# Performance work log

Hardware: AMD Instinct MI355X
Metric: run time of the kernel (lower is better)

## Reference

```python
import jax, jax.numpy as jnp
import numpy as np

NEG_SLOPE = 0.2  # PyG GATConv default leaky_relu slope


def gat_conv(h_in, src, dst, W, a_src, a_dst, b, N):
    # h_in: [N, Fin]; src/dst: [E] (self-loops already appended)
    h = h_in @ W                      # [N, Fout]
    alpha_src = h @ a_src             # [N]
    alpha_dst = h @ a_dst             # [N]
    e = jax.nn.leaky_relu(alpha_src[src] + alpha_dst[dst], NEG_SLOPE)  # [E]
    # segment softmax over incoming edges of each destination node
    m = jax.ops.segment_max(e, dst, num_segments=N)
    m = jnp.where(jnp.isfinite(m), m, 0.0)
    p = jnp.exp(e - m[dst])
    denom = jax.ops.segment_sum(p, dst, num_segments=N)
    alpha = p / jnp.maximum(denom[dst], 1e-16)
    out = jax.ops.segment_sum(alpha[:, None] * h[src], dst, num_segments=N)
    return out + b


def setup_inputs() -> dict:
    key = jax.random.key(0)
    ks = jax.random.split(key, 16)
    N, E, V, D, H, C, G = 100000, 1600000, 128, 50, 16, 10, 512
    x = jax.random.normal(ks[0], (N, V), dtype=jnp.float32)
    edge_index = jax.random.randint(ks[1], (2, E), 0, N, dtype=jnp.int32)
    batch = jnp.sort(jax.random.randint(ks[2], (N,), 0, G, dtype=jnp.int32))
    s = lambda fan: 1.0 / np.sqrt(fan)
    return {
        "x": x, "edge_index": edge_index, "batch": batch,
        "embedding": jax.random.normal(ks[3], (V, D), dtype=jnp.float32),
        "W1": jax.random.normal(ks[4], (D, H), dtype=jnp.float32) * s(D),
        "a_src1": jax.random.normal(ks[5], (H,), dtype=jnp.float32) * s(H),
        "a_dst1": jax.random.normal(ks[6], (H,), dtype=jnp.float32) * s(H),
        "b1": jnp.zeros((H,), dtype=jnp.float32),
        "W2": jax.random.normal(ks[7], (H, H), dtype=jnp.float32) * s(H),
        "a_src2": jax.random.normal(ks[8], (H,), dtype=jnp.float32) * s(H),
        "a_dst2": jax.random.normal(ks[9], (H,), dtype=jnp.float32) * s(H),
        "b2": jnp.zeros((H,), dtype=jnp.float32),
        "W3": jax.random.normal(ks[10], (H, C), dtype=jnp.float32) * s(H),
        "a_src3": jax.random.normal(ks[11], (C,), dtype=jnp.float32) * s(C),
        "a_dst3": jax.random.normal(ks[12], (C,), dtype=jnp.float32) * s(C),
        "b3": jnp.zeros((C,), dtype=jnp.float32),
    }


def reference(x, edge_index, batch, embedding, W1, a_src1, a_dst1, b1,
              W2, a_src2, a_dst2, b2, W3, a_src3, a_dst3, b3):
    N = x.shape[0]
    G = 512  # num graphs
    # embedding lookup via argmax over one-hot-ish features
    idx = jnp.argmax(x, axis=1)
    h = embedding[idx]                               # [N, 50]
    # add self-loops once (PyG GATConv default)
    loops = jnp.arange(N, dtype=edge_index.dtype)
    src = jnp.concatenate([edge_index[0], loops])
    dst = jnp.concatenate([edge_index[1], loops])
    h = jax.nn.relu(gat_conv(h, src, dst, W1, a_src1, a_dst1, b1, N))
    # dropout: eval mode -> identity
    h = jax.nn.relu(gat_conv(h, src, dst, W2, a_src2, a_dst2, b2, N))
    h = gat_conv(h, src, dst, W3, a_src3, a_dst3, b3, N)  # [N, C]
    # global mean pool over graphs
    sums = jax.ops.segment_sum(h, batch, num_segments=G)
    cnts = jax.ops.segment_sum(jnp.ones((N,), h.dtype), batch, num_segments=G)
    pooled = sums / jnp.maximum(cnts, 1.0)[:, None]
    return jax.nn.softmax(pooled, axis=1)
```

## Files before the change

kernel.cpp:

```cpp
#include <hip/hip_runtime.h>
#include <math.h>

#define NEG_SLOPE 0.2f
#define NBUK_MAX 512

typedef float v4f __attribute__((ext_vector_type(4)));

template <int B2>
__global__ void __launch_bounds__(1024)
k_histarg(const float* __restrict__ x, const int* __restrict__ edst, int E,
          int* __restrict__ histT, int NBUK, int* __restrict__ idx, int N, int V) {
    __shared__ int sh[NBUK_MAX];
    int t = threadIdx.x;
    if ((int)blockIdx.x < B2) {
        int b = blockIdx.x;
        for (int k = t; k < NBUK; k += 1024) sh[k] = 0;
        __syncthreads();
        long long ebeg = (long long)b * E / B2, eend = (long long)(b + 1) * E / B2;
        for (long long i = ebeg + t; i < eend; i += 1024)
            atomicAdd(&sh[edst[i] >> 8], 1);
        __syncthreads();
        for (int k = t; k < NBUK; k += 1024) histT[(long long)k * B2 + b] = sh[k];
    } else {
        int node = ((int)blockIdx.x - B2) * 32 + (t >> 5);
        int lane = t & 31;
        if (node >= N) return;
        const v4f* row = (const v4f*)(x + (long long)node * V);
        float bv = -INFINITY;
        int bi = 0x7fffffff;
        int nq = V >> 2;
        for (int q = lane; q < nq; q += 32) {
            v4f v = row[q];
            int base = q << 2;
            if (v.x > bv || (v.x == bv && base     < bi)) { bv = v.x; bi = base;     }
            if (v.y > bv || (v.y == bv && base + 1 < bi)) { bv = v.y; bi = base + 1; }
            if (v.z > bv || (v.z == bv && base + 2 < bi)) { bv = v.z; bi = base + 2; }
            if (v.w > bv || (v.w == bv && base + 3 < bi)) { bv = v.w; bi = base + 3; }
        }
        for (int off = 16; off > 0; off >>= 1) {
            float ov = __shfl_down(bv, off, 32);
            int   oi = __shfl_down(bi, off, 32);
            if (ov > bv || (ov == bv && oi < bi)) { bv = ov; bi = oi; }
        }
        if (lane == 0) idx[node] = bi;
    }
}

template <int FIN, int FOUT>
__global__ void __launch_bounds__(256)
k_scan_tr(const int* __restrict__ vals, int* __restrict__ excl, int* __restrict__ bsums, int M,
          const float* __restrict__ emb, const int* __restrict__ idx,
          const float* __restrict__ W, const float* __restrict__ a_src,
          const float* __restrict__ a_dst, _Float16* __restrict__ h_t,
          float* __restrict__ asrc, float* __restrict__ adst, int N, int NB_SCAN) {
    __shared__ int s[256];
    __shared__ float sW[FIN * FOUT];
    __shared__ float sa[FOUT], sd[FOUT];
    int t = threadIdx.x;
    if ((int)blockIdx.x < NB_SCAN) {
        int i = blockIdx.x * 256 + t;
        int v = (i < M) ? vals[i] : 0;
        s[t] = v;
        __syncthreads();
        for (int off = 1; off < 256; off <<= 1) {
            int a = (t >= off) ? s[t - off] : 0;
            __syncthreads();
            s[t] += a;
            __syncthreads();
        }
        if (i < M) excl[i] = s[t] - v;
        if (t == 255) bsums[blockIdx.x] = s[255];
    } else {
        for (int i = t; i < FIN * FOUT; i += 256) sW[i] = W[i];
        if (t < FOUT) { sa[t] = a_src[t]; sd[t] = a_dst[t]; }
        __syncthreads();
        int n = ((int)blockIdx.x - NB_SCAN) * 256 + t;
        if (n >= N) return;
        float acc[FOUT];
#pragma unroll
        for (int f = 0; f < FOUT; f++) acc[f] = 0.f;
        const float* hr = emb + (long long)idx[n] * FIN;
        for (int k = 0; k < FIN; k++) {
            float v = hr[k];
#pragma unroll
            for (int f = 0; f < FOUT; f++) acc[f] += v * sW[k * FOUT + f];
        }
        float s1 = 0.f, s2 = 0.f;
        _Float16 hh[16];
#pragma unroll
        for (int f = 0; f < 16; f++) hh[f] = (_Float16)0.f;
#pragma unroll
        for (int f = 0; f < FOUT; f++) {
            hh[f] = (_Float16)acc[f];
            s1 += acc[f] * sa[f];
            s2 += acc[f] * sd[f];
        }
        uint4* dst = (uint4*)(h_t + (long long)n * 16);
        dst[0] = ((uint4*)hh)[0];
        dst[1] = ((uint4*)hh)[1];
        asrc[n] = s1;
        adst[n] = s2;
    }
}

__global__ void k_scan2(int* __restrict__ bsums, int nb) {
    __shared__ int s[2048];
    int i = threadIdx.x;
    int v0 = (i < nb) ? bsums[i] : 0;
    int v1 = (i + 1024 < nb) ? bsums[i + 1024] : 0;
    s[i] = v0;
    s[i + 1024] = v1;
    __syncthreads();
    for (int off = 1; off < 2048; off <<= 1) {
        int a0 = (i >= off) ? s[i - off] : 0;
        int a1 = (i + 1024 >= off) ? s[i + 1024 - off] : 0;
        __syncthreads();
        s[i] += a0;
        s[i + 1024] += a1;
        __syncthreads();
    }
    if (i < nb) bsums[i] = s[i] - v0;
    if (i + 1024 < nb) bsums[i + 1024] = s[i + 1024] - v1;
}

template <int B2>
__global__ void __launch_bounds__(1024)
k_scatB(const int* __restrict__ esrc, const int* __restrict__ edst, int E,
        const int* __restrict__ sexcl, const int* __restrict__ bsums,
        int* __restrict__ tmp, int NBUK) {
    __shared__ int cur[NBUK_MAX];
    int t = threadIdx.x, b = blockIdx.x;
    for (int k = t; k < NBUK; k += 1024)
        cur[k] = sexcl[(long long)k * B2 + b] + bsums[k];
    __syncthreads();
    long long ebeg = (long long)b * E / B2, eend = (long long)(b + 1) * E / B2;
    for (long long i = ebeg + t; i < eend; i += 1024) {
        int d = edst[i];
        int pos = atomicAdd(&cur[d >> 8], 1);
        tmp[pos] = ((d & 255) << 17) | esrc[i];
    }
}

template <int B2>
__global__ void __launch_bounds__(256)
k_binB(const int* __restrict__ sexcl, const int* __restrict__ bsums,
       const int* __restrict__ tmp,
       int* __restrict__ rowptr, int* __restrict__ csr_src, int N, int NBUK, int E) {
    __shared__ int cnt[256];
    __shared__ int scn[256];
    __shared__ int cur[256];
    int t = threadIdx.x, b = blockIdx.x;
    int t0 = sexcl[(long long)b * B2] + bsums[b];
    int t1 = (b + 1 < NBUK) ? (sexcl[(long long)(b + 1) * B2] + bsums[b + 1]) : E;
    cnt[t] = 0;
    __syncthreads();
    for (int i = t0 + t; i < t1; i += 256) atomicAdd(&cnt[tmp[i] >> 17], 1);
    __syncthreads();
    int v = cnt[t];
    scn[t] = v;
    __syncthreads();
    for (int off = 1; off < 256; off <<= 1) {
        int a = (t >= off) ? scn[t - off] : 0;
        __syncthreads();
        scn[t] += a;
        __syncthreads();
    }
    int base = t0 + scn[t] - v;
    int d = (b << 8) + t;
    if (d < N) rowptr[d] = base;
    cur[t] = base;
    if (d == N - 1) rowptr[N] = E;
    __syncthreads();
    for (int i = t0 + t; i < t1; i += 256) {
        int p = tmp[i];
        int pos = atomicAdd(&cur[p >> 17], 1);
        csr_src[pos] = p & 0x1FFFF;
    }
}

template <typename EPI>
__device__ __forceinline__ void gat_core(const int* __restrict__ rowptr,
                                         const int* __restrict__ csr_src,
                                         const float* __restrict__ asrc,
                                         const float* __restrict__ adst,
                                         const _Float16* __restrict__ h_t,
                                         int N, int grp, int lane, EPI epilogue) {
    int d = grp;
    int r0 = rowptr[d], r1 = rowptr[d + 1];
    float ad = adst[d];

    float e0 = asrc[d] + ad;
    e0 = (e0 >= 0.f) ? e0 : NEG_SLOPE * e0;
    float p0 = __expf(e0);
    float acc  = p0 * (float)h_t[(long long)d * 16 + lane];
    float psum = (lane == 0) ? p0 : 0.f;

    int j = r0;
    if (j < r1) {
        int myj = j + lane;
        bool valid = myj < r1;
        int s = valid ? csr_src[myj] : d;
        float a = asrc[s];
        while (true) {
            int jn = j + 16;
            int s2 = d; float a2 = 0.f; bool validn = false;
            if (jn < r1) {
                int myjn = jn + lane;
                validn = myjn < r1;
                s2 = validn ? csr_src[myjn] : d;
                a2 = asrc[s2];
            }
            float e = a + ad;
            e = (e >= 0.f) ? e : NEG_SLOPE * e;
            float p = valid ? __expf(e) : 0.f;
            psum += p;
#pragma unroll
            for (int k = 0; k < 16; k++) {
                float pk = __shfl(p, k, 16);
                int   sk = __shfl(s, k, 16);
                acc += pk * (float)h_t[(long long)sk * 16 + lane];
            }
            if (jn >= r1) break;
            j = jn; s = s2; a = a2; valid = validn;
        }
    }
    for (int off = 8; off > 0; off >>= 1) psum += __shfl_xor(psum, off, 16);
    epilogue(d, acc / fmaxf(psum, 1e-16f));
}

template <int FN>
__global__ void k_gat_ft(const int* __restrict__ rowptr, const int* __restrict__ csr_src,
                         const float* __restrict__ asrc, const float* __restrict__ adst,
                         const _Float16* __restrict__ h_t, const float* __restrict__ bias,
                         const float* __restrict__ Wn, const float* __restrict__ an_src,
                         const float* __restrict__ an_dst,
                         _Float16* __restrict__ h_next, float* __restrict__ asrc_n,
                         float* __restrict__ adst_n, int N) {
    __shared__ float sW[16 * FN];
    __shared__ float sa[FN], sd[FN], sb[16];
    for (int i = threadIdx.x; i < 16 * FN; i += blockDim.x) sW[i] = Wn[i];
    if (threadIdx.x < FN) { sa[threadIdx.x] = an_src[threadIdx.x]; sd[threadIdx.x] = an_dst[threadIdx.x]; }
    if (threadIdx.x < 16) sb[threadIdx.x] = bias[threadIdx.x];
    __syncthreads();

    int grp  = (blockIdx.x * blockDim.x + threadIdx.x) >> 4;
    int lane = threadIdx.x & 15;
    if (grp >= N) return;

    gat_core(rowptr, csr_src, asrc, adst, h_t, N, grp, lane,
        [&](int d, float v) {
            v = fmaxf(v + sb[lane], 0.f);
            float acc2 = 0.f;
#pragma unroll
            for (int k = 0; k < 16; k++) {
                float vk = __shfl(v, k, 16);
                if (lane < FN) acc2 += vk * sW[k * FN + lane];
            }
            float c1 = (lane < FN) ? acc2 * sa[lane] : 0.f;
            float c2 = (lane < FN) ? acc2 * sd[lane] : 0.f;
            for (int off = 8; off > 0; off >>= 1) {
                c1 += __shfl_xor(c1, off, 16);
                c2 += __shfl_xor(c2, off, 16);
            }
            h_next[(long long)d * 16 + lane] = (_Float16)((lane < FN) ? acc2 : 0.f);
            if (lane == 0) { asrc_n[d] = c1; adst_n[d] = c2; }
        });
}

template <int FOUT>
__global__ void k_gat_last(const int* __restrict__ rowptr, const int* __restrict__ csr_src,
                           const float* __restrict__ asrc, const float* __restrict__ adst,
                           const _Float16* __restrict__ h_t, float* __restrict__ out, int N) {
    int grp  = (blockIdx.x * blockDim.x + threadIdx.x) >> 4;
    int lane = threadIdx.x & 15;
    if (grp >= N) return;
    gat_core(rowptr, csr_src, asrc, adst, h_t, N, grp, lane,
        [&](int d, float v) {
            if (lane < FOUT) out[(long long)d * FOUT + lane] = v;
        });
}

__global__ void k_pool(const float* __restrict__ h3, const int* __restrict__ batch,
                       const float* __restrict__ b3, float* __restrict__ out, int N, int C) {
    int g = blockIdx.x;
    int lo = 0, hi = N;
    while (lo < hi) { int mid = (lo + hi) >> 1; if (batch[mid] < g) lo = mid + 1; else hi = mid; }
    int start = lo;
    hi = N;
    while (lo < hi) { int mid = (lo + hi) >> 1; if (batch[mid] < g + 1) lo = mid + 1; else hi = mid; }
    int end = lo;

    float sum[16];
    for (int f = 0; f < C; f++) sum[f] = 0.f;
    for (int n = start + threadIdx.x; n < end; n += blockDim.x) {
        const float* r = h3 + (long long)n * C;
        for (int f = 0; f < C; f++) sum[f] += r[f];
    }
    __shared__ float red[256 * 16];
    for (int f = 0; f < C; f++) red[threadIdx.x * 16 + f] = sum[f];
    __syncthreads();
    for (int str = blockDim.x / 2; str > 0; str >>= 1) {
        if ((int)threadIdx.x < str)
            for (int f = 0; f < C; f++) red[threadIdx.x * 16 + f] += red[(threadIdx.x + str) * 16 + f];
        __syncthreads();
    }
    if (threadIdx.x == 0) {
        float cnt = fmaxf((float)(end - start), 1.f);
        float vals[16];
        float mx = -INFINITY;
        for (int f = 0; f < C; f++) { vals[f] = red[f] / cnt + b3[f]; mx = fmaxf(mx, vals[f]); }
        float se = 0.f;
        for (int f = 0; f < C; f++) { vals[f] = __expf(vals[f] - mx); se += vals[f]; }
        for (int f = 0; f < C; f++) out[(long long)g * C + f] = vals[f] / se;
    }
}

extern "C" void kernel_launch(void* const* d_in, const int* in_sizes, int n_in,
                              void* d_out, int out_size, void* d_ws, size_t ws_size,
                              hipStream_t stream) {
    const float* x    = (const float*)d_in[0];
    const int*   eidx = (const int*)d_in[1];
    const int*   batch= (const int*)d_in[2];
    const float* emb  = (const float*)d_in[3];
    const float* W1   = (const float*)d_in[4];
    const float* as1  = (const float*)d_in[5];
    const float* ad1  = (const float*)d_in[6];
    const float* b1   = (const float*)d_in[7];
    const float* W2   = (const float*)d_in[8];
    const float* as2  = (const float*)d_in[9];
    const float* ad2  = (const float*)d_in[10];
    const float* b2   = (const float*)d_in[11];
    const float* W3   = (const float*)d_in[12];
    const float* as3  = (const float*)d_in[13];
    const float* ad3  = (const float*)d_in[14];
    const float* b3   = (const float*)d_in[15];

    const int H = in_sizes[5];
    const int C = in_sizes[13];
    const int D = in_sizes[4] / H;
    const int V = in_sizes[3] / D;
    const int N = in_sizes[0] / V;
    const int E = in_sizes[1] / 2;
    const int G = out_size / C;
    const int* esrc = eidx;
    const int* edst = eidx + E;
    const int NBUK = (N + 255) >> 8;
    constexpr int B2 = 256;
    const int M = NBUK * B2;

    char* w = (char*)d_ws;
    auto carve = [&](size_t bytes) {
        char* p = w;
        w += (bytes + 255) & ~(size_t)255;
        return p;
    };
    float*     as_a    = (float*)carve((size_t)N * 4);
    float*     ad_a    = (float*)carve((size_t)N * 4);
    float*     as_b    = (float*)carve((size_t)N * 4);
    float*     ad_b    = (float*)carve((size_t)N * 4);
    int*       idx     = (int*)carve((size_t)N * 4);
    int*       rowptr  = (int*)carve((size_t)(N + 1) * 4);
    int*       csr_src = (int*)carve((size_t)E * 4);
    int*       histT   = (int*)carve((size_t)M * 4);
    int*       sexcl   = (int*)carve((size_t)M * 4);
    int*       bsums   = (int*)carve(2048 * 4);
    _Float16*  hTa     = (_Float16*)carve((size_t)N * 16 * 2);
    _Float16*  hTb     = (_Float16*)carve((size_t)N * 16 * 2);
    size_t zone_bytes = ((size_t)E * 4 > (size_t)N * C * 4) ? (size_t)E * 4 : (size_t)N * C * 4;
    char*  zone = carve(zone_bytes);
    float* X0  = (float*)zone;
    int*   tmp = (int*)zone;
    (void)ws_size; (void)n_in;

    const int BT = 256;
    dim3 blk(BT);
    int gGat  = (N * 16 + BT - 1) / BT;
    int nb2   = (M + 255) / 256;
    int gArg  = (N + 31) / 32;
    int gTr   = (N + BT - 1) / BT;

    k_histarg<B2><<<B2 + gArg, dim3(1024), 0, stream>>>(x, edst, E, histT, NBUK, idx, N, V);

    k_scan_tr<50, 16><<<nb2 + gTr, blk, 0, stream>>>(histT, sexcl, bsums, M,
                                                     emb, idx, W1, as1, ad1, hTa, as_a, ad_a, N, nb2);
    k_scan2<<<1, 1024, 0, stream>>>(bsums, nb2);

    k_scatB<B2><<<B2, dim3(1024), 0, stream>>>(esrc, edst, E, sexcl, bsums, tmp, NBUK);
    k_binB<B2><<<NBUK, blk, 0, stream>>>(sexcl, bsums, tmp, rowptr, csr_src, N, NBUK, E);

    k_gat_ft<16><<<gGat, blk, 0, stream>>>(rowptr, csr_src, as_a, ad_a, hTa, b1,
                                           W2, as2, ad2, hTb, as_b, ad_b, N);

    k_gat_ft<10><<<gGat, blk, 0, stream>>>(rowptr, csr_src, as_b, ad_b, hTb, b2,
                                           W3, as3, ad3, hTa, as_a, ad_a, N);

    k_gat_last<10><<<gGat, blk, 0, stream>>>(rowptr, csr_src, as_a, ad_a, hTa, X0, N);

    k_pool<<<G, blk, 0, stream>>>(X0, batch, b3, (float*)d_out, N, C);
}
```

Baseline: 266.4 us.

## Use 4 lanes per node with half4 gathers in GAT layers; fold bucket scan

The GAT aggregation kernels now assign 4 lanes per destination node instead of 16. Each lane gathers a packed half4 of features and processes edges in chunks of 4, which cuts wasted lanes for low-degree nodes (average degree about 17) and raises bytes per load. The separate single-block k_scan2 launch is removed; k_scatB and k_binB each redo the small bucket-sum scan in shared memory. The epilogue matmul is restructured to 4 outputs per lane, and the final output is padded to 16 floats per node, which costs more memory for X0 and for the pool reads.

```diff
diff --git a/kernel.cpp b/kernel.cpp
--- a/kernel.cpp
+++ b/kernel.cpp
@@ -5,6 +5,7 @@
 #define NBUK_MAX 512
 
 typedef float v4f __attribute__((ext_vector_type(4)));
+typedef _Float16 h4v __attribute__((ext_vector_type(4)));
 
 template <int B2>
 __global__ void __launch_bounds__(1024)
@@ -103,35 +104,24 @@
     }
 }
 
-__global__ void k_scan2(int* __restrict__ bsums, int nb) {
-    __shared__ int s[2048];
-    int i = threadIdx.x;
-    int v0 = (i < nb) ? bsums[i] : 0;
-    int v1 = (i + 1024 < nb) ? bsums[i + 1024] : 0;
-    s[i] = v0;
-    s[i + 1024] = v1;
-    __syncthreads();
-    for (int off = 1; off < 2048; off <<= 1) {
-        int a0 = (i >= off) ? s[i - off] : 0;
-        int a1 = (i + 1024 >= off) ? s[i + 1024 - off] : 0;
-        __syncthreads();
-        s[i] += a0;
-        s[i + 1024] += a1;
-        __syncthreads();
-    }
-    if (i < nb) bsums[i] = s[i] - v0;
-    if (i + 1024 < nb) bsums[i + 1024] = s[i + 1024] - v1;
-}
-
 template <int B2>
 __global__ void __launch_bounds__(1024)
 k_scatB(const int* __restrict__ esrc, const int* __restrict__ edst, int E,
         const int* __restrict__ sexcl, const int* __restrict__ bsums,
         int* __restrict__ tmp, int NBUK) {
     __shared__ int cur[NBUK_MAX];
+    __shared__ int bex[512];
     int t = threadIdx.x, b = blockIdx.x;
+    if (t < 512) bex[t] = (t < NBUK) ? bsums[t] : 0;
+    __syncthreads();
+    for (int off = 1; off < 512; off <<= 1) {
+        int a = (t < 512 && t >= off) ? bex[t - off] : 0;
+        __syncthreads();
+        if (t < 512) bex[t] += a;
+        __syncthreads();
+    }
     for (int k = t; k < NBUK; k += 1024)
-        cur[k] = sexcl[(long long)k * B2 + b] + bsums[k];
+        cur[k] = sexcl[(long long)k * B2 + b] + (k ? bex[k - 1] : 0);
     __syncthreads();
     long long ebeg = (long long)b * E / B2, eend = (long long)(b + 1) * E / B2;
     for (long long i = ebeg + t; i < eend; i += 1024) {
@@ -146,12 +136,24 @@
 k_binB(const int* __restrict__ sexcl, const int* __restrict__ bsums,
        const int* __restrict__ tmp,
        int* __restrict__ rowptr, int* __restrict__ csr_src, int N, int NBUK, int E) {
+    __shared__ int bx[512];
     __shared__ int cnt[256];
     __shared__ int scn[256];
     __shared__ int cur[256];
     int t = threadIdx.x, b = blockIdx.x;
-    int t0 = sexcl[(long long)b * B2] + bsums[b];
-    int t1 = (b + 1 < NBUK) ? (sexcl[(long long)(b + 1) * B2] + bsums[b + 1]) : E;
+    bx[t]       = (t < NBUK)       ? bsums[t]       : 0;
+    bx[t + 256] = (t + 256 < NBUK) ? bsums[t + 256] : 0;
+    __syncthreads();
+    for (int off = 1; off < 512; off <<= 1) {
+        int a0 = (t >= off) ? bx[t - off] : 0;
+        int a1 = (t + 256 >= off) ? bx[t + 256 - off] : 0;
+        __syncthreads();
+        bx[t] += a0;
+        bx[t + 256] += a1;
+        __syncthreads();
+    }
+    int t0 = sexcl[(long long)b * B2] + (b ? bx[b - 1] : 0);
+    int t1 = (b + 1 < NBUK) ? (sexcl[(long long)(b + 1) * B2] + bx[b]) : E;
     cnt[t] = 0;
     __syncthreads();
     for (int i = t0 + t; i < t1; i += 256) atomicAdd(&cnt[tmp[i] >> 17], 1);
@@ -179,104 +181,129 @@
 }
 
 template <typename EPI>
-__device__ __forceinline__ void gat_core(const int* __restrict__ rowptr,
-                                         const int* __restrict__ csr_src,
-                                         const float* __restrict__ asrc,
-                                         const float* __restrict__ adst,
-                                         const _Float16* __restrict__ h_t,
-                                         int N, int grp, int lane, EPI epilogue) {
-    int d = grp;
+__device__ __forceinline__ void gat_core4(const int* __restrict__ rowptr,
+                                          const int* __restrict__ csr_src,
+                                          const float* __restrict__ asrc,
+                                          const float* __restrict__ adst,
+                                          const _Float16* __restrict__ h_t,
+                                          int d, int l4, EPI epilogue) {
+    const h4v* __restrict__ H = (const h4v*)h_t;
     int r0 = rowptr[d], r1 = rowptr[d + 1];
     float ad = adst[d];
 
     float e0 = asrc[d] + ad;
     e0 = (e0 >= 0.f) ? e0 : NEG_SLOPE * e0;
     float p0 = __expf(e0);
-    float acc  = p0 * (float)h_t[(long long)d * 16 + lane];
-    float psum = (lane == 0) ? p0 : 0.f;
-
-    int j = r0;
-    if (j < r1) {
-        int myj = j + lane;
-        bool valid = myj < r1;
-        int s = valid ? csr_src[myj] : d;
-        float a = asrc[s];
+    h4v hd = H[(long long)d * 4 + l4];
+    float a0 = p0 * (float)hd[0], a1 = p0 * (float)hd[1];
+    float a2 = p0 * (float)hd[2], a3 = p0 * (float)hd[3];
+    float psum = (l4 == 0) ? p0 : 0.f;
+
+    int rem = r1 - r0;
+    if (rem > 0) {
+        int j = r0;
+        int s = (l4 < rem) ? csr_src[j + l4] : d;
+        float av = asrc[s];
         while (true) {
-            int jn = j + 16;
-            int s2 = d; float a2 = 0.f; bool validn = false;
-            if (jn < r1) {
-                int myjn = jn + lane;
-                validn = myjn < r1;
-                s2 = validn ? csr_src[myjn] : d;
-                a2 = asrc[s2];
+            int remn = rem - 4;
+            int s2 = d; float av2 = 0.f;
+            if (remn > 0) {
+                s2 = (l4 < remn) ? csr_src[j + 4 + l4] : d;
+                av2 = asrc[s2];
             }
-            float e = a + ad;
+            float e = av + ad;
             e = (e >= 0.f) ? e : NEG_SLOPE * e;
-            float p = valid ? __expf(e) : 0.f;
+            float p = (l4 < rem) ? __expf(e) : 0.f;
             psum += p;
 #pragma unroll
-            for (int k = 0; k < 16; k++) {
-                float pk = __shfl(p, k, 16);
-                int   sk = __shfl(s, k, 16);
-                acc += pk * (float)h_t[(long long)sk * 16 + lane];
+            for (int k = 0; k < 4; k++) {
+                float pk = __shfl(p, k, 4);
+                int   sk = __shfl(s, k, 4);
+                h4v hh = H[(long long)sk * 4 + l4];
+                a0 += pk * (float)hh[0];
+                a1 += pk * (float)hh[1];
+                a2 += pk * (float)hh[2];
+                a3 += pk * (float)hh[3];
             }
-            if (jn >= r1) break;
-            j = jn; s = s2; a = a2; valid = validn;
-        }
-    }
-    for (int off = 8; off > 0; off >>= 1) psum += __shfl_xor(psum, off, 16);
-    epilogue(d, acc / fmaxf(psum, 1e-16f));
+            if (remn <= 0) break;
+            j += 4; rem = remn; s = s2; av = av2;
+        }
+    }
+    psum += __shfl_xor(psum, 1, 4);
+    psum += __shfl_xor(psum, 2, 4);
+    float inv = 1.f / fmaxf(psum, 1e-16f);
+    epilogue(d, a0 * inv, a1 * inv, a2 * inv, a3 * inv);
 }
 
 template <int FN>
-__global__ void k_gat_ft(const int* __restrict__ rowptr, const int* __restrict__ csr_src,
-                         const float* __restrict__ asrc, const float* __restrict__ adst,
-                         const _Float16* __restrict__ h_t, const float* __restrict__ bias,
-                         const float* __restrict__ Wn, const float* __restrict__ an_src,
-                         const float* __restrict__ an_dst,
-                         _Float16* __restrict__ h_next, float* __restrict__ asrc_n,
-                         float* __restrict__ adst_n, int N) {
-    __shared__ float sW[16 * FN];
-    __shared__ float sa[FN], sd[FN], sb[16];
-    for (int i = threadIdx.x; i < 16 * FN; i += blockDim.x) sW[i] = Wn[i];
-    if (threadIdx.x < FN) { sa[threadIdx.x] = an_src[threadIdx.x]; sd[threadIdx.x] = an_dst[threadIdx.x]; }
-    if (threadIdx.x < 16) sb[threadIdx.x] = bias[threadIdx.x];
-    __syncthreads();
-
-    int grp  = (blockIdx.x * blockDim.x + threadIdx.x) >> 4;
-    int lane = threadIdx.x & 15;
-    if (grp >= N) return;
-
-    gat_core(rowptr, csr_src, asrc, adst, h_t, N, grp, lane,
-        [&](int d, float v) {
-            v = fmaxf(v + sb[lane], 0.f);
-            float acc2 = 0.f;
-#pragma unroll
-            for (int k = 0; k < 16; k++) {
-                float vk = __shfl(v, k, 16);
-                if (lane < FN) acc2 += vk * sW[k * FN + lane];
+__global__ void __launch_bounds__(256)
+k_gat_ft(const int* __restrict__ rowptr, const int* __restrict__ csr_src,
+         const float* __restrict__ asrc, const float* __restrict__ adst,
+         const _Float16* __restrict__ h_t, const float* __restrict__ bias,
+         const float* __restrict__ Wn, const float* __restrict__ an_src,
+         const float* __restrict__ an_dst,
+         _Float16* __restrict__ h_next, float* __restrict__ asrc_n,
+         float* __restrict__ adst_n, int N) {
+    __shared__ float sW[16 * 16];
+    __shared__ float sa[16], sd[16], sb[16];
+    int t = threadIdx.x;
+    {
+        int k = t >> 4, f = t & 15;
+        sW[t] = (f < FN) ? Wn[k * FN + f] : 0.f;
+    }
+    if (t < 16) {
+        sa[t] = (t < FN) ? an_src[t] : 0.f;
+        sd[t] = (t < FN) ? an_dst[t] : 0.f;
+        sb[t] = bias[t];
+    }
+    __syncthreads();
+
+    int gid = blockIdx.x * 256 + t;
+    int d = gid >> 2, l4 = gid & 3;
+    if (d >= N) return;
+
+    gat_core4(rowptr, csr_src, asrc, adst, h_t, d, l4,
+        [&](int dd, float v0, float v1, float v2, float v3) {
+            int f0 = l4 * 4;
+            float vv[4];
+            vv[0] = fmaxf(v0 + sb[f0    ], 0.f);
+            vv[1] = fmaxf(v1 + sb[f0 + 1], 0.f);
+            vv[2] = fmaxf(v2 + sb[f0 + 2], 0.f);
+            vv[3] = fmaxf(v3 + sb[f0 + 3], 0.f);
+            float o0 = 0.f, o1 = 0.f, o2 = 0.f, o3 = 0.f;
+#pragma unroll
+            for (int q = 0; q < 4; q++) {
+#pragma unroll
+                for (int i = 0; i < 4; i++) {
+                    float vk = __shfl(vv[i], q, 4);
+                    const float* wr = &sW[(q * 4 + i) * 16 + f0];
+                    o0 += vk * wr[0];
+                    o1 += vk * wr[1];
+                    o2 += vk * wr[2];
+                    o3 += vk * wr[3];
+                }
             }
-            float c1 = (lane < FN) ? acc2 * sa[lane] : 0.f;
-            float c2 = (lane < FN) ? acc2 * sd[lane] : 0.f;
-            for (int off = 8; off > 0; off >>= 1) {
-                c1 += __shfl_xor(c1, off, 16);
-                c2 += __shfl_xor(c2, off, 16);
-            }
-            h_next[(long long)d * 16 + lane] = (_Float16)((lane < FN) ? acc2 : 0.f);
-            if (lane == 0) { asrc_n[d] = c1; adst_n[d] = c2; }
+            float c1 = o0 * sa[f0] + o1 * sa[f0 + 1] + o2 * sa[f0 + 2] + o3 * sa[f0 + 3];
+            float c2 = o0 * sd[f0] + o1 * sd[f0 + 1] + o2 * sd[f0 + 2] + o3 * sd[f0 + 3];
+            c1 += __shfl_xor(c1, 1, 4); c1 += __shfl_xor(c1, 2, 4);
+            c2 += __shfl_xor(c2, 1, 4); c2 += __shfl_xor(c2, 2, 4);
+            h4v ho = { (_Float16)o0, (_Float16)o1, (_Float16)o2, (_Float16)o3 };
+            ((h4v*)h_next)[(long long)dd * 4 + l4] = ho;
+            if (l4 == 0) { asrc_n[dd] = c1; adst_n[dd] = c2; }
         });
 }
 
-template <int FOUT>
-__global__ void k_gat_last(const int* __restrict__ rowptr, const int* __restrict__ csr_src,
-                           const float* __restrict__ asrc, const float* __restrict__ adst,
-                           const _Float16* __restrict__ h_t, float* __restrict__ out, int N) {
-    int grp  = (blockIdx.x * blockDim.x + threadIdx.x) >> 4;
-    int lane = threadIdx.x & 15;
-    if (grp >= N) return;
-    gat_core(rowptr, csr_src, asrc, adst, h_t, N, grp, lane,
-        [&](int d, float v) {
-            if (lane < FOUT) out[(long long)d * FOUT + lane] = v;
+__global__ void __launch_bounds__(256)
+k_gat_last(const int* __restrict__ rowptr, const int* __restrict__ csr_src,
+           const float* __restrict__ asrc, const float* __restrict__ adst,
+           const _Float16* __restrict__ h_t, float* __restrict__ out, int N) {
+    int gid = blockIdx.x * 256 + threadIdx.x;
+    int d = gid >> 2, l4 = gid & 3;
+    if (d >= N) return;
+    gat_core4(rowptr, csr_src, asrc, adst, h_t, d, l4,
+        [&](int dd, float v0, float v1, float v2, float v3) {
+            v4f o = { v0, v1, v2, v3 };
+            ((v4f*)out)[(long long)dd * 4 + l4] = o;
         });
 }
 
@@ -293,7 +320,7 @@
     float sum[16];
     for (int f = 0; f < C; f++) sum[f] = 0.f;
     for (int n = start + threadIdx.x; n < end; n += blockDim.x) {
-        const float* r = h3 + (long long)n * C;
+        const float* r = h3 + (long long)n * 16;
         for (int f = 0; f < C; f++) sum[f] += r[f];
     }
     __shared__ float red[256 * 16];
@@ -366,7 +393,7 @@
     int*       bsums   = (int*)carve(2048 * 4);
     _Float16*  hTa     = (_Float16*)carve((size_t)N * 16 * 2);
     _Float16*  hTb     = (_Float16*)carve((size_t)N * 16 * 2);
-    size_t zone_bytes = ((size_t)E * 4 > (size_t)N * C * 4) ? (size_t)E * 4 : (size_t)N * C * 4;
+    size_t zone_bytes = ((size_t)E * 4 > (size_t)N * 64) ? (size_t)E * 4 : (size_t)N * 64;
     char*  zone = carve(zone_bytes);
     float* X0  = (float*)zone;
     int*   tmp = (int*)zone;
@@ -374,7 +401,7 @@
 
     const int BT = 256;
     dim3 blk(BT);
-    int gGat  = (N * 16 + BT - 1) / BT;
+    int gGat4 = (N * 4 + BT - 1) / BT;
     int nb2   = (M + 255) / 256;
     int gArg  = (N + 31) / 32;
     int gTr   = (N + BT - 1) / BT;
@@ -383,18 +410,17 @@
 
     k_scan_tr<50, 16><<<nb2 + gTr, blk, 0, stream>>>(histT, sexcl, bsums, M,
                                                      emb, idx, W1, as1, ad1, hTa, as_a, ad_a, N, nb2);
-    k_scan2<<<1, 1024, 0, stream>>>(bsums, nb2);
 
     k_scatB<B2><<<B2, dim3(1024), 0, stream>>>(esrc, edst, E, sexcl, bsums, tmp, NBUK);
     k_binB<B2><<<NBUK, blk, 0, stream>>>(sexcl, bsums, tmp, rowptr, csr_src, N, NBUK, E);
 
-    k_gat_ft<16><<<gGat, blk, 0, stream>>>(rowptr, csr_src, as_a, ad_a, hTa, b1,
-                                           W2, as2, ad2, hTb, as_b, ad_b, N);
-
-    k_gat_ft<10><<<gGat, blk, 0, stream>>>(rowptr, csr_src, as_b, ad_b, hTb, b2,
-                                           W3, as3, ad3, hTa, as_a, ad_a, N);
-
-    k_gat_last<10><<<gGat, blk, 0, stream>>>(rowptr, csr_src, as_a, ad_a, hTa, X0, N);
+    k_gat_ft<16><<<gGat4, blk, 0, stream>>>(rowptr, csr_src, as_a, ad_a, hTa, b1,
+                                            W2, as2, ad2, hTb, as_b, ad_b, N);
+
+    k_gat_ft<10><<<gGat4, blk, 0, stream>>>(rowptr, csr_src, as_b, ad_b, hTb, b2,
+                                            W3, as3, ad3, hTa, as_a, ad_a, N);
+
+    k_gat_last<<<gGat4, blk, 0, stream>>>(rowptr, csr_src, as_a, ad_a, hTa, X0, N);
 
     k_pool<<<G, blk, 0, stream>>>(X0, batch, b3, (float*)d_out, N, C);
 }
```

Result: faster. 254.6 us (-4.4%).
